# Kernel tuning notes

Hardware: AMD Instinct MI355X
Metric: run time of the kernel (lower is better)

Reference implementation:

```python
import jax, jax.numpy as jnp
import numpy as np
import math

D_MODEL = 1024
N_HEADS = 16
D_K = D_MODEL // N_HEADS
SEQ_LEN = 2048
BATCH = 2


def setup_inputs() -> dict:
    key = jax.random.key(0)
    ks = jax.random.split(key, 5)
    X = jax.random.normal(ks[0], (BATCH, SEQ_LEN, D_MODEL), dtype=jnp.float32)
    # Linear params (torch Linear: y = x @ W.T + b). Store as [in, out] for einsum.
    sc1 = 1.0 / math.sqrt(D_MODEL)
    W_qkv = jax.random.uniform(ks[1], (D_MODEL, 3 * D_MODEL), jnp.float32, -sc1, sc1)
    b_qkv = jax.random.uniform(ks[2], (3 * D_MODEL,), jnp.float32, -sc1, sc1)
    W_out = jax.random.uniform(ks[3], (D_MODEL, D_MODEL), jnp.float32, -sc1, sc1)
    b_out = jax.random.uniform(ks[4], (D_MODEL,), jnp.float32, -sc1, sc1)
    return {"X": X, "W_qkv": W_qkv, "b_qkv": b_qkv, "W_out": W_out, "b_out": b_out}


def reference(X, W_qkv, b_qkv, W_out, b_out):
    B, S, E = X.shape
    qkv = X @ W_qkv + b_qkv                       # [B,S,3E]
    qkv = qkv.reshape(B, S, 3, N_HEADS, D_K)
    q = jnp.transpose(qkv[:, :, 0], (0, 2, 1, 3))  # [B,H,S,Dk]
    k = jnp.transpose(qkv[:, :, 1], (0, 2, 1, 3))
    v = jnp.transpose(qkv[:, :, 2], (0, 2, 1, 3))
    scores = jnp.einsum('bhqd,bhkd->bhqk', q, k) / math.sqrt(D_K)
    causal = jnp.tril(jnp.ones((S, S), dtype=bool))
    scores = jnp.where(causal[None, None], scores, -jnp.inf)
    probs = jax.nn.softmax(scores, axis=-1)
    out = jnp.einsum('bhqk,bhkd->bhqd', probs, v)  # [B,H,S,Dk]
    out = jnp.transpose(out, (0, 2, 1, 3)).reshape(B, S, E)
    return out @ W_out + b_out
```

## Files before the change

kernel.cpp:

```cpp
#include <hip/hip_runtime.h>

typedef __bf16 bf16_t;
typedef bf16_t bf16x8 __attribute__((ext_vector_type(8)));
typedef bf16_t bf16x4 __attribute__((ext_vector_type(4)));
typedef float f32x4 __attribute__((ext_vector_type(4)));

#define SEQLEN 2048
#define EMB 1024
#define NHEADS 16
#define N3 3072
#define NBATCH 2
#define NEG_INF (-__builtin_inff())
#define SC2 0.18033688011112042f

__device__ __forceinline__ void async16(bf16_t* lds, const bf16_t* g) {
    __builtin_amdgcn_global_load_lds(
        (const __attribute__((address_space(1))) void*)g,
        (__attribute__((address_space(3))) void*)lds, 16, 0, 0);
}

__global__ __launch_bounds__(256) void prep_kernel(
    const float* __restrict__ X, const float* __restrict__ Wqkv,
    const float* __restrict__ Wout, bf16_t* __restrict__ Xb,
    bf16_t* __restrict__ Wqkv_t, bf16_t* __restrict__ Wout_t)
{
    __shared__ float tile[64][65];
    const int id = blockIdx.x;
    const int t = threadIdx.x;
    if (id < 2048) {
        const int i = (id * 256 + t) * 8;
        float4 a = *(const float4*)&X[i];
        float4 b = *(const float4*)&X[i + 4];
        bf16_t v[8];
        v[0] = (bf16_t)a.x; v[1] = (bf16_t)a.y; v[2] = (bf16_t)a.z; v[3] = (bf16_t)a.w;
        v[4] = (bf16_t)b.x; v[5] = (bf16_t)b.y; v[6] = (bf16_t)b.z; v[7] = (bf16_t)b.w;
        *(float4*)&Xb[i] = *(float4*)&v[0];
        return;
    }
    const int wid2 = id - 2048;
    int bx = wid2 & 63;
    const int k0 = (wid2 >> 6) << 6;
    const float* W; bf16_t* Wt; int N; float s;
    if (bx < 48) { W = Wqkv; Wt = Wqkv_t; N = N3;  s = (bx * 64 < EMB) ? SC2 : 1.0f; }
    else         { bx -= 48; W = Wout; Wt = Wout_t; N = EMB; s = 1.0f; }
    const int n0 = bx * 64;
    const int nl = t & 63, k4 = t >> 6;
#pragma unroll
    for (int i = 0; i < 16; ++i) {
        int kk = k4 + i * 4;
        tile[kk][nl] = W[(size_t)(k0 + kk) * N + n0 + nl];
    }
    __syncthreads();
    const int kl = t & 63, n4 = t >> 6;
#pragma unroll
    for (int i = 0; i < 16; ++i) {
        int nn = n4 + i * 4;
        Wt[(size_t)(n0 + nn) * EMB + k0 + kl] = (bf16_t)(tile[kl][nn] * s);
    }
}

template<bool OUT_BF16, bool V_SPLIT>
__global__ __launch_bounds__(256) void gemm_bt_kernel(
    const bf16_t* __restrict__ A, const bf16_t* __restrict__ Bt,
    const float* __restrict__ bias, void* __restrict__ Cp,
    bf16_t* __restrict__ vt, int scale_q,
    int Mdim, int Ndim, int Kdim)
{
    __shared__ bf16_t As[128 * 64];
    __shared__ bf16_t Bs[128 * 64];
    const int nb = Ndim >> 7;
    const int cpx = gridDim.x >> 3;
    const int bid = (blockIdx.x & 7) * cpx + (blockIdx.x >> 3);
    const int bx = bid % nb, by = bid / nb;
    const int r0 = by << 7, c0 = bx << 7;
    const int t = threadIdx.x, lane = t & 63;
    const int wid = t >> 6;
    const int wm = wid >> 1, wn = wid & 1;
    const int lr = lane & 15, lg = lane >> 4;

    const int glrow = wid * 32 + (lane >> 3);
    const int gsw = ((lane & 7) ^ (lane >> 3)) << 3;
    const bf16_t* gA = &A[(size_t)(r0 + glrow) * Kdim + gsw];
    const bf16_t* gB = &Bt[(size_t)(c0 + glrow) * Kdim + gsw];
    bf16_t* ldsA = &As[wid * 2048];
    bf16_t* ldsB = &Bs[wid * 2048];
    const size_t row8 = (size_t)8 * Kdim;

    const int fragb0 = (lr * 128 + lg * 16) ^ ((lr & 7) << 4);
    const int fragb1 = (lr * 128 + 64 + lg * 16) ^ ((lr & 7) << 4);

    f32x4 acc[4][4] = {};
    const int KT = Kdim >> 6;
    for (int kt = 0; kt < KT; ++kt) {
        const bf16_t* a = gA + kt * 64;
        const bf16_t* b = gB + kt * 64;
        async16(ldsA,        a);
        async16(ldsA + 512,  a + row8);
        async16(ldsA + 1024, a + 2 * row8);
        async16(ldsA + 1536, a + 3 * row8);
        async16(ldsB,        b);
        async16(ldsB + 512,  b + row8);
        async16(ldsB + 1024, b + 2 * row8);
        async16(ldsB + 1536, b + 3 * row8);
        __syncthreads();

        const char* Ab = (const char*)As + wm * 8192;
        const char* Bb = (const char*)Bs + wn * 8192;
        bf16x8 af[4], bfm[4];
#pragma unroll
        for (int m = 0; m < 4; ++m)
            af[m] = *(const bf16x8*)(Ab + m * 2048 + fragb0);
#pragma unroll
        for (int n = 0; n < 4; ++n)
            bfm[n] = *(const bf16x8*)(Bb + n * 2048 + fragb0);
#pragma unroll
        for (int m = 0; m < 4; ++m)
#pragma unroll
            for (int n = 0; n < 4; ++n)
                acc[m][n] = __builtin_amdgcn_mfma_f32_16x16x32_bf16(
                    af[m], bfm[n], acc[m][n], 0, 0, 0);
#pragma unroll
        for (int m = 0; m < 4; ++m)
            af[m] = *(const bf16x8*)(Ab + m * 2048 + fragb1);
#pragma unroll
        for (int n = 0; n < 4; ++n)
            bfm[n] = *(const bf16x8*)(Bb + n * 2048 + fragb1);
#pragma unroll
        for (int m = 0; m < 4; ++m)
#pragma unroll
            for (int n = 0; n < 4; ++n)
                acc[m][n] = __builtin_amdgcn_mfma_f32_16x16x32_bf16(
                    af[m], bfm[n], acc[m][n], 0, 0, 0);
        __syncthreads();
    }

    const bool vmode = V_SPLIT && (c0 >= 2 * EMB);
    const int lgp = ((lg & 1) << 1) | (lg >> 1);
#pragma unroll
    for (int m = 0; m < 4; ++m) {
#pragma unroll
        for (int n = 0; n < 4; ++n) {
            const int col = c0 + wn * 64 + n * 16 + lr;
            float bval = bias[col];
            if (scale_q && col < EMB) bval *= SC2;
            if (vmode) {
                const int h = (col - 2 * EMB) >> 6, dd = col & 63;
                const int bb = r0 >> 11;
                const int sbase = (r0 & (SEQLEN - 1)) + wm * 64 + m * 16 + lgp * 4;
                bf16x4 pk;
#pragma unroll
                for (int j = 0; j < 4; ++j) pk[j] = (bf16_t)(acc[m][n][j] + bval);
                *(bf16x4*)&vt[(size_t)((bb * 16 + h) * 64 + dd) * SEQLEN + sbase] = pk;
            } else {
#pragma unroll
                for (int j = 0; j < 4; ++j) {
                    const int row = r0 + wm * 64 + m * 16 + lg * 4 + j;
                    const float v = acc[m][n][j] + bval;
                    if (OUT_BF16)
                        ((bf16_t*)Cp)[(size_t)row * Ndim + col] = (bf16_t)v;
                    else
                        ((float*)Cp)[(size_t)row * Ndim + col] = v;
                }
            }
        }
    }
}

__global__ __launch_bounds__(512, 4) void attn_kernel(
    const bf16_t* __restrict__ qkv, const bf16_t* __restrict__ vt,
    bf16_t* __restrict__ attn_out)
{
    __shared__ bf16_t Kl[2][8192];
    __shared__ bf16_t Vl[2][8192];
    const int d = blockIdx.x;
    const int r = d >> 8;
    const int u = (d >> 5) & 7;
    const int bh = d & 31;
    const int qt = r ? u : (15 - u);
    const int b = bh >> 4, h = bh & 15;
    const int q0 = qt << 7;
    const int t = threadIdx.x, lane = t & 63, wid = t >> 6;
    const int lr = lane & 15, lg = lane >> 4;

    const int kfb0 = (lr * 128 + lg * 16) ^ ((lr & 7) << 4);
    const int kfb1 = (lr * 128 + 64 + lg * 16) ^ ((lr & 7) << 4);
    const int vfb0 = (lr * 256 + lg * 16) ^ ((lr & 7) << 4);
    const int vfb1 = (lr * 256 + 64 + lg * 16) ^ ((lr & 7) << 4);
    const int vfb2 = (lr * 256 + 128 + lg * 16) ^ ((lr & 7) << 4);
    const int vfb3 = (lr * 256 + 192 + lg * 16) ^ ((lr & 7) << 4);

    const int srk = t >> 3, sck = (t & 7) << 3;
    const int srv = t >> 4, scv = (t & 15) << 3;
    const int stbK = (srk * 128 + sck * 2) ^ ((srk & 7) << 4);
    const int stbV = (srv * 256 + scv * 2) ^ ((srv & 7) << 4);

    const bf16_t* kp = &qkv[(size_t)(b * SEQLEN + srk) * N3 + EMB + h * 64 + sck];
    const bf16_t* vp = &vt[(size_t)(bh * 64 + srv) * SEQLEN + scv];
    const size_t kstep  = (size_t)128 * N3;
    const size_t krow64 = (size_t)64 * N3;
    const size_t vrow32 = (size_t)32 * SEQLEN;

    const int qb = q0 + wid * 16;
    const int qg = qb + lr;
    bf16x8 qa0, qa1;
    {
        const bf16_t* qp = &qkv[(size_t)(b * SEQLEN + qg) * N3 + h * 64];
        qa0 = *(const bf16x8*)&qp[lg * 8];
        qa1 = *(const bf16x8*)&qp[32 + lg * 8];
    }
    bf16x8 ones;
#pragma unroll
    for (int i = 0; i < 8; ++i) ones[i] = (bf16_t)1.0f;

    f32x4 o[4] = {};
    f32x4 ol = {};
    float m_run = NEG_INF;

    auto stage = [&](int buf, float4 k0, float4 k1, float4 v0, float4 v1) {
        char* K = (char*)Kl[buf]; char* V = (char*)Vl[buf];
        *(float4*)(K + stbK) = k0; *(float4*)(K + stbK + 8192) = k1;
        *(float4*)(V + stbV) = v0; *(float4*)(V + stbV + 8192) = v1;
    };

    {
        float4 k0 = *(const float4*)kp, k1 = *(const float4*)(kp + krow64);
        float4 v0 = *(const float4*)vp, v1 = *(const float4*)(vp + vrow32);
        stage(0, k0, k1, v0, v1);
    }
    __syncthreads();
    int cur = 0;
    for (int kt = 0; kt <= qt; ++kt) {
        float4 nk0, nk1, nv0, nv1;
        const bool more = (kt < qt);
        if (more) {
            kp += kstep; vp += 128;
            nk0 = *(const float4*)kp; nk1 = *(const float4*)(kp + krow64);
            nv0 = *(const float4*)vp; nv1 = *(const float4*)(vp + vrow32);
        }

        const char* Kc = (const char*)Kl[cur];
        const char* Vc = (const char*)Vl[cur];
        const int kbase = kt << 7;

        f32x4 sc[8] = {};
        __builtin_amdgcn_s_setprio(1);
#pragma unroll
        for (int n = 0; n < 8; ++n) {
            bf16x8 kb0 = *(const bf16x8*)(Kc + (kfb0 + n * 2048));
            bf16x8 kb1 = *(const bf16x8*)(Kc + (kfb1 + n * 2048));
            sc[n] = __builtin_amdgcn_mfma_f32_16x16x32_bf16(kb0, qa0, sc[n], 0, 0, 0);
            sc[n] = __builtin_amdgcn_mfma_f32_16x16x32_bf16(kb1, qa1, sc[n], 0, 0, 0);
        }
        __builtin_amdgcn_s_setprio(0);

        if (kt == qt) {
#pragma unroll
            for (int n = 0; n < 8; ++n)
#pragma unroll
                for (int j = 0; j < 4; ++j) {
                    const int kg = kbase + n * 16 + lg * 4 + j;
                    sc[n][j] = (kg <= qg) ? sc[n][j] : NEG_INF;
                }
        }
        float mx[8];
#pragma unroll
        for (int n = 0; n < 8; ++n)
            mx[n] = fmaxf(fmaxf(fmaxf(sc[n][0], sc[n][1]), sc[n][2]), sc[n][3]);
        float pmax = fmaxf(
            fmaxf(fmaxf(mx[0], mx[1]), fmaxf(mx[2], mx[3])),
            fmaxf(fmaxf(mx[4], mx[5]), fmaxf(mx[6], mx[7])));

        if (__any(pmax > m_run + 8.f)) {
            float pm = fmaxf(pmax, __shfl_xor(pmax, 16));
            pm = fmaxf(pm, __shfl_xor(pm, 32));
            const float mnew = fmaxf(m_run, pm);
            const float alpha = exp2f(m_run - mnew);
            m_run = mnew;
            float al[4];
#pragma unroll
            for (int j = 0; j < 4; ++j) al[j] = __shfl(alpha, lg * 4 + j);
#pragma unroll
            for (int dn = 0; dn < 4; ++dn)
#pragma unroll
                for (int j = 0; j < 4; ++j) o[dn][j] *= al[j];
#pragma unroll
            for (int j = 0; j < 4; ++j) ol[j] *= al[j];
        }

#pragma unroll
        for (int n = 0; n < 8; ++n)
#pragma unroll
            for (int j = 0; j < 4; ++j) sc[n][j] = exp2f(sc[n][j] - m_run);

        union UW { unsigned w[4]; bf16x8 v; };
        bf16x8 pa0, pa1, pa2, pa3;
        {
            unsigned pk00, pk01, pk10, pk11, pk20, pk21, pk30, pk31;
            asm("v_cvt_pk_bf16_f32 %0, %1, %2" : "=v"(pk00) : "v"(sc[0][0]), "v"(sc[0][1]));
            asm("v_cvt_pk_bf16_f32 %0, %1, %2" : "=v"(pk01) : "v"(sc[0][2]), "v"(sc[0][3]));
            asm("v_cvt_pk_bf16_f32 %0, %1, %2" : "=v"(pk10) : "v"(sc[1][0]), "v"(sc[1][1]));
            asm("v_cvt_pk_bf16_f32 %0, %1, %2" : "=v"(pk11) : "v"(sc[1][2]), "v"(sc[1][3]));
            asm("v_cvt_pk_bf16_f32 %0, %1, %2" : "=v"(pk20) : "v"(sc[2][0]), "v"(sc[2][1]));
            asm("v_cvt_pk_bf16_f32 %0, %1, %2" : "=v"(pk21) : "v"(sc[2][2]), "v"(sc[2][3]));
            asm("v_cvt_pk_bf16_f32 %0, %1, %2" : "=v"(pk30) : "v"(sc[3][0]), "v"(sc[3][1]));
            asm("v_cvt_pk_bf16_f32 %0, %1, %2" : "=v"(pk31) : "v"(sc[3][2]), "v"(sc[3][3]));
            asm("v_permlane32_swap_b32 %0, %1" : "+v"(pk00), "+v"(pk10));
            asm("v_permlane32_swap_b32 %0, %1" : "+v"(pk01), "+v"(pk11));
            asm("v_permlane32_swap_b32 %0, %1" : "+v"(pk20), "+v"(pk30));
            asm("v_permlane32_swap_b32 %0, %1" : "+v"(pk21), "+v"(pk31));
            UW ua, ub;
            ua.w[0] = pk00; ua.w[1] = pk01; ua.w[2] = pk10; ua.w[3] = pk11;
            ub.w[0] = pk20; ub.w[1] = pk21; ub.w[2] = pk30; ub.w[3] = pk31;
            pa0 = ua.v; pa1 = ub.v;
        }
        {
            unsigned pk00, pk01, pk10, pk11, pk20, pk21, pk30, pk31;
            asm("v_cvt_pk_bf16_f32 %0, %1, %2" : "=v"(pk00) : "v"(sc[4][0]), "v"(sc[4][1]));
            asm("v_cvt_pk_bf16_f32 %0, %1, %2" : "=v"(pk01) : "v"(sc[4][2]), "v"(sc[4][3]));
            asm("v_cvt_pk_bf16_f32 %0, %1, %2" : "=v"(pk10) : "v"(sc[5][0]), "v"(sc[5][1]));
            asm("v_cvt_pk_bf16_f32 %0, %1, %2" : "=v"(pk11) : "v"(sc[5][2]), "v"(sc[5][3]));
            asm("v_cvt_pk_bf16_f32 %0, %1, %2" : "=v"(pk20) : "v"(sc[6][0]), "v"(sc[6][1]));
            asm("v_cvt_pk_bf16_f32 %0, %1, %2" : "=v"(pk21) : "v"(sc[6][2]), "v"(sc[6][3]));
            asm("v_cvt_pk_bf16_f32 %0, %1, %2" : "=v"(pk30) : "v"(sc[7][0]), "v"(sc[7][1]));
            asm("v_cvt_pk_bf16_f32 %0, %1, %2" : "=v"(pk31) : "v"(sc[7][2]), "v"(sc[7][3]));
            asm("v_permlane32_swap_b32 %0, %1" : "+v"(pk00), "+v"(pk10));
            asm("v_permlane32_swap_b32 %0, %1" : "+v"(pk01), "+v"(pk11));
            asm("v_permlane32_swap_b32 %0, %1" : "+v"(pk20), "+v"(pk30));
            asm("v_permlane32_swap_b32 %0, %1" : "+v"(pk21), "+v"(pk31));
            UW ua, ub;
            ua.w[0] = pk00; ua.w[1] = pk01; ua.w[2] = pk10; ua.w[3] = pk11;
            ub.w[0] = pk20; ub.w[1] = pk21; ub.w[2] = pk30; ub.w[3] = pk31;
            pa2 = ua.v; pa3 = ub.v;
        }

        __builtin_amdgcn_s_setprio(1);
#pragma unroll
        for (int dn = 0; dn < 4; ++dn) {
            bf16x8 vb0 = *(const bf16x8*)(Vc + (vfb0 + dn * 4096));
            bf16x8 vb1 = *(const bf16x8*)(Vc + (vfb1 + dn * 4096));
            bf16x8 vb2 = *(const bf16x8*)(Vc + (vfb2 + dn * 4096));
            bf16x8 vb3 = *(const bf16x8*)(Vc + (vfb3 + dn * 4096));
            o[dn] = __builtin_amdgcn_mfma_f32_16x16x32_bf16(pa0, vb0, o[dn], 0, 0, 0);
            o[dn] = __builtin_amdgcn_mfma_f32_16x16x32_bf16(pa1, vb1, o[dn], 0, 0, 0);
            o[dn] = __builtin_amdgcn_mfma_f32_16x16x32_bf16(pa2, vb2, o[dn], 0, 0, 0);
            o[dn] = __builtin_amdgcn_mfma_f32_16x16x32_bf16(pa3, vb3, o[dn], 0, 0, 0);
        }
        ol = __builtin_amdgcn_mfma_f32_16x16x32_bf16(pa0, ones, ol, 0, 0, 0);
        ol = __builtin_amdgcn_mfma_f32_16x16x32_bf16(pa1, ones, ol, 0, 0, 0);
        ol = __builtin_amdgcn_mfma_f32_16x16x32_bf16(pa2, ones, ol, 0, 0, 0);
        ol = __builtin_amdgcn_mfma_f32_16x16x32_bf16(pa3, ones, ol, 0, 0, 0);
        __builtin_amdgcn_s_setprio(0);

        if (more) {
            stage(cur ^ 1, nk0, nk1, nv0, nv1);
        }
        __syncthreads();
        cur ^= 1;
    }

    float li[4];
#pragma unroll
    for (int j = 0; j < 4; ++j) li[j] = 1.0f / ol[j];
#pragma unroll
    for (int dn = 0; dn < 4; ++dn)
#pragma unroll
        for (int j = 0; j < 4; ++j) {
            const int row = b * SEQLEN + qb + lg * 4 + j;
            attn_out[(size_t)row * EMB + h * 64 + dn * 16 + lr] =
                (bf16_t)(o[dn][j] * li[j]);
        }
}

extern "C" void kernel_launch(void* const* d_in, const int* in_sizes, int n_in,
                              void* d_out, int out_size, void* d_ws, size_t ws_size,
                              hipStream_t stream)
{
    const float* X     = (const float*)d_in[0];
    const float* W_qkv = (const float*)d_in[1];
    const float* b_qkv = (const float*)d_in[2];
    const float* W_out = (const float*)d_in[3];
    const float* b_out = (const float*)d_in[4];
    float* out = (float*)d_out;

    char* ws = (char*)d_ws;
    bf16_t* Wqkv_t = (bf16_t*)ws;
    bf16_t* Wout_t = (bf16_t*)(ws + 6u * 1024 * 1024);
    bf16_t* qkv    = (bf16_t*)(ws + 8u * 1024 * 1024);
    bf16_t* attn   = (bf16_t*)(ws + 32u * 1024 * 1024);
    bf16_t* Xb     = (bf16_t*)(ws + 40u * 1024 * 1024);
    bf16_t* Vt_g   = (bf16_t*)(ws + 48u * 1024 * 1024);

    dim3 blk(256);
    prep_kernel<<<3072, blk, 0, stream>>>(X, W_qkv, W_out, Xb, Wqkv_t, Wout_t);

    gemm_bt_kernel<true, true><<<(4096 / 128) * (N3 / 128), blk, 0, stream>>>(
        Xb, Wqkv_t, b_qkv, (void*)qkv, Vt_g, 1, 4096, N3, EMB);

    attn_kernel<<<512, dim3(512), 0, stream>>>(qkv, Vt_g, attn);

    gemm_bt_kernel<false, false><<<(4096 / 128) * (EMB / 128), blk, 0, stream>>>(
        attn, Wout_t, b_out, (void*)out, nullptr, 0, 4096, EMB, EMB);
}
```

Baseline: 103.4 us.

## Double-buffer GEMM LDS tiles with async prefetch and relayout attention V tile

The GEMM kernel now keeps two LDS buffers for A and B and issues the async global-to-LDS loads for tile kt+2 while tile kt+1 is in flight. It uses explicit vmcnt waits and raw s_barrier in place of the full __syncthreads per iteration, so global load latency can overlap MFMA work. Separately, the attention kernel stores the V tile as two 64-column halves with 128-byte rows and the same XOR swizzle as K, which is meant to cut LDS bank conflicts on V fragment reads. The GEMM change doubles LDS use, which may lower occupancy, and the hand-placed waitcnt logic depends on exact load counts being correct.

```diff
diff --git a/kernel.cpp b/kernel.cpp
--- a/kernel.cpp
+++ b/kernel.cpp
@@ -12,6 +12,11 @@
 #define NBATCH 2
 #define NEG_INF (-__builtin_inff())
 #define SC2 0.18033688011112042f
+
+#define VMC8() do { asm volatile("s_waitcnt vmcnt(8)" ::: "memory"); \
+                    __builtin_amdgcn_sched_barrier(0); } while (0)
+#define VMC0() do { asm volatile("s_waitcnt vmcnt(0)" ::: "memory"); \
+                    __builtin_amdgcn_sched_barrier(0); } while (0)
 
 __device__ __forceinline__ void async16(bf16_t* lds, const bf16_t* g) {
     __builtin_amdgcn_global_load_lds(
@@ -66,8 +71,8 @@
     bf16_t* __restrict__ vt, int scale_q,
     int Mdim, int Ndim, int Kdim)
 {
-    __shared__ bf16_t As[128 * 64];
-    __shared__ bf16_t Bs[128 * 64];
+    __shared__ bf16_t As[2][128 * 64];
+    __shared__ bf16_t Bs[2][128 * 64];
     const int nb = Ndim >> 7;
     const int cpx = gridDim.x >> 3;
     const int bid = (blockIdx.x & 7) * cpx + (blockIdx.x >> 3);
@@ -82,30 +87,37 @@
     const int gsw = ((lane & 7) ^ (lane >> 3)) << 3;
     const bf16_t* gA = &A[(size_t)(r0 + glrow) * Kdim + gsw];
     const bf16_t* gB = &Bt[(size_t)(c0 + glrow) * Kdim + gsw];
-    bf16_t* ldsA = &As[wid * 2048];
-    bf16_t* ldsB = &Bs[wid * 2048];
     const size_t row8 = (size_t)8 * Kdim;
 
     const int fragb0 = (lr * 128 + lg * 16) ^ ((lr & 7) << 4);
     const int fragb1 = (lr * 128 + 64 + lg * 16) ^ ((lr & 7) << 4);
 
+    auto stage = [&](int buf, int kt) {
+        const bf16_t* a = gA + kt * 64;
+        const bf16_t* b = gB + kt * 64;
+        bf16_t* dA = &As[buf][wid * 2048];
+        bf16_t* dB = &Bs[buf][wid * 2048];
+        async16(dA,        a);
+        async16(dA + 512,  a + row8);
+        async16(dA + 1024, a + 2 * row8);
+        async16(dA + 1536, a + 3 * row8);
+        async16(dB,        b);
+        async16(dB + 512,  b + row8);
+        async16(dB + 1024, b + 2 * row8);
+        async16(dB + 1536, b + 3 * row8);
+    };
+
     f32x4 acc[4][4] = {};
     const int KT = Kdim >> 6;
+
+    stage(0, 0);
+    if (KT > 1) { stage(1, 1); VMC8(); } else { VMC0(); }
+    __builtin_amdgcn_s_barrier();
+
     for (int kt = 0; kt < KT; ++kt) {
-        const bf16_t* a = gA + kt * 64;
-        const bf16_t* b = gB + kt * 64;
-        async16(ldsA,        a);
-        async16(ldsA + 512,  a + row8);
-        async16(ldsA + 1024, a + 2 * row8);
-        async16(ldsA + 1536, a + 3 * row8);
-        async16(ldsB,        b);
-        async16(ldsB + 512,  b + row8);
-        async16(ldsB + 1024, b + 2 * row8);
-        async16(ldsB + 1536, b + 3 * row8);
-        __syncthreads();
-
-        const char* Ab = (const char*)As + wm * 8192;
-        const char* Bb = (const char*)Bs + wn * 8192;
+        const int cur = kt & 1;
+        const char* Ab = (const char*)&As[cur][0] + wm * 8192;
+        const char* Bb = (const char*)&Bs[cur][0] + wn * 8192;
         bf16x8 af[4], bfm[4];
 #pragma unroll
         for (int m = 0; m < 4; ++m)
@@ -131,7 +143,11 @@
             for (int n = 0; n < 4; ++n)
                 acc[m][n] = __builtin_amdgcn_mfma_f32_16x16x32_bf16(
                     af[m], bfm[n], acc[m][n], 0, 0, 0);
-        __syncthreads();
+
+        __builtin_amdgcn_s_barrier();
+        if (kt + 2 < KT) { stage(cur, kt + 2); VMC8(); }
+        else if (kt + 1 < KT) { VMC0(); }
+        __builtin_amdgcn_s_barrier();
     }
 
     const bool vmode = V_SPLIT && (c0 >= 2 * EMB);
@@ -184,15 +200,12 @@
 
     const int kfb0 = (lr * 128 + lg * 16) ^ ((lr & 7) << 4);
     const int kfb1 = (lr * 128 + 64 + lg * 16) ^ ((lr & 7) << 4);
-    const int vfb0 = (lr * 256 + lg * 16) ^ ((lr & 7) << 4);
-    const int vfb1 = (lr * 256 + 64 + lg * 16) ^ ((lr & 7) << 4);
-    const int vfb2 = (lr * 256 + 128 + lg * 16) ^ ((lr & 7) << 4);
-    const int vfb3 = (lr * 256 + 192 + lg * 16) ^ ((lr & 7) << 4);
 
     const int srk = t >> 3, sck = (t & 7) << 3;
     const int srv = t >> 4, scv = (t & 15) << 3;
     const int stbK = (srk * 128 + sck * 2) ^ ((srk & 7) << 4);
-    const int stbV = (srv * 256 + scv * 2) ^ ((srv & 7) << 4);
+    const int stbV = (((srv * 128 + (scv & 63) * 2) ^ ((srv & 7) << 4)))
+                     + ((scv >> 6) << 13);
 
     const bf16_t* kp = &qkv[(size_t)(b * SEQLEN + srk) * N3 + EMB + h * 64 + sck];
     const bf16_t* vp = &vt[(size_t)(bh * 64 + srv) * SEQLEN + scv];
@@ -219,7 +232,7 @@
     auto stage = [&](int buf, float4 k0, float4 k1, float4 v0, float4 v1) {
         char* K = (char*)Kl[buf]; char* V = (char*)Vl[buf];
         *(float4*)(K + stbK) = k0; *(float4*)(K + stbK + 8192) = k1;
-        *(float4*)(V + stbV) = v0; *(float4*)(V + stbV + 8192) = v1;
+        *(float4*)(V + stbV) = v0; *(float4*)(V + stbV + 4096) = v1;
     };
 
     {
@@ -336,10 +349,10 @@
         __builtin_amdgcn_s_setprio(1);
 #pragma unroll
         for (int dn = 0; dn < 4; ++dn) {
-            bf16x8 vb0 = *(const bf16x8*)(Vc + (vfb0 + dn * 4096));
-            bf16x8 vb1 = *(const bf16x8*)(Vc + (vfb1 + dn * 4096));
-            bf16x8 vb2 = *(const bf16x8*)(Vc + (vfb2 + dn * 4096));
-            bf16x8 vb3 = *(const bf16x8*)(Vc + (vfb3 + dn * 4096));
+            bf16x8 vb0 = *(const bf16x8*)(Vc + (kfb0 + dn * 2048));
+            bf16x8 vb1 = *(const bf16x8*)(Vc + (kfb1 + dn * 2048));
+            bf16x8 vb2 = *(const bf16x8*)(Vc + (kfb0 + dn * 2048 + 8192));
+            bf16x8 vb3 = *(const bf16x8*)(Vc + (kfb1 + dn * 2048 + 8192));
             o[dn] = __builtin_amdgcn_mfma_f32_16x16x32_bf16(pa0, vb0, o[dn], 0, 0, 0);
             o[dn] = __builtin_amdgcn_mfma_f32_16x16x32_bf16(pa1, vb1, o[dn], 0, 0, 0);
             o[dn] = __builtin_amdgcn_mfma_f32_16x16x32_bf16(pa2, vb2, o[dn], 0, 0, 0);
```

After: 111.6 us. 7.8% more time.
